# Kernel optimization log

Measured on AMD Instinct MI355X. Metric: run time of the kernel, lower is better.

## Reference

```python
import jax, jax.numpy as jnp
import numpy as np

N, C, H, E = 10000, 128, 256, 320000
CUTOFF = 5.0
EPS = 1e-5


def _ln(x, g, b):
    mu = jnp.mean(x, axis=-1, keepdims=True)
    var = jnp.var(x, axis=-1, keepdims=True)
    return (x - mu) * jax.lax.rsqrt(var + EPS) * g + b


def setup_inputs() -> dict:
    key = jax.random.key(0)
    ks = jax.random.split(key, 24)

    def w(k, shape, fan_in):
        return (jax.random.normal(k, shape, dtype=jnp.float32) / np.sqrt(fan_in)).astype(jnp.float32)

    inp = {}
    inp["x"] = jax.random.normal(ks[0], (N, 3), dtype=jnp.float32)
    inp["h"] = jax.random.normal(ks[1], (N, C), dtype=jnp.float32)
    inp["edge_index"] = jax.random.randint(ks[2], (2, E), 0, N, dtype=jnp.int32)
    # edge_mlp: Linear(2C+1 -> H), SiLU, Linear(H -> H), SiLU
    inp["We1"] = w(ks[3], (2 * C + 1, H), 2 * C + 1); inp["be1"] = jnp.zeros((H,), jnp.float32)
    inp["We2"] = w(ks[4], (H, H), H);                inp["be2"] = jnp.zeros((H,), jnp.float32)
    # node_mlp: Linear(C+H -> H), SiLU, Linear(H -> C)
    inp["Wn1"] = w(ks[5], (C + H, H), C + H);        inp["bn1"] = jnp.zeros((H,), jnp.float32)
    inp["Wn2"] = w(ks[6], (H, C), H);                inp["bn2"] = jnp.zeros((C,), jnp.float32)
    # residual mlp: Linear(C -> H), SiLU, Dropout(eval), Linear(H -> C)
    inp["Wm1"] = w(ks[7], (C, H), C);                inp["bm1"] = jnp.zeros((H,), jnp.float32)
    inp["Wm2"] = w(ks[8], (H, C), H);                inp["bm2"] = jnp.zeros((C,), jnp.float32)
    # layernorms
    inp["g1"] = jnp.ones((C,), jnp.float32); inp["beta1"] = jnp.zeros((C,), jnp.float32)
    inp["g2"] = jnp.ones((C,), jnp.float32); inp["beta2"] = jnp.zeros((C,), jnp.float32)
    return inp


def reference(x, h, edge_index, We1, be1, We2, be2, Wn1, bn1, Wn2, bn2,
              Wm1, bm1, Wm2, bm2, g1, beta1, g2, beta2):
    row, col = edge_index[0], edge_index[1]

    h_res = h
    hn = _ln(h, g1, beta1)                              # [N, C]

    # ---- EGNN layer ----
    rel = x[row] - x[col]                               # [E, 3]
    dist = jnp.linalg.norm(rel, axis=-1, keepdims=True) # [E, 1]
    edge_in = jnp.concatenate([hn[row], hn[col], dist], axis=-1)  # [E, 2C+1]
    m = jax.nn.silu(edge_in @ We1 + be1)
    m = jax.nn.silu(m @ We2 + be2)                      # [E, H]

    d = dist[:, 0]
    Ccut = 0.5 * (jnp.cos(d * jnp.pi / CUTOFF) + 1.0)
    Ccut = Ccut * (d <= CUTOFF) * (d >= 0.0)
    m = m * Ccut[:, None]

    # mean-aggregate messages at target nodes (edge_index[1])
    sums = jax.ops.segment_sum(m, col, num_segments=N)          # [N, H]
    cnt = jax.ops.segment_sum(jnp.ones((m.shape[0],), m.dtype), col, num_segments=N)
    m_aggr = sums / jnp.maximum(cnt, 1.0)[:, None]

    hd = jax.nn.silu(jnp.concatenate([hn, m_aggr], axis=-1) @ Wn1 + bn1) @ Wn2 + bn2
    h_egnn = hn + hd

    h1 = h_res + h_egnn

    # ---- norm2 + MLP residual (dropout = identity in eval) ----
    h2 = _ln(h1, g2, beta2)
    h2 = jax.nn.silu(h2 @ Wm1 + bm1) @ Wm2 + bm2
    return h1 + h2
```

## Files before the change

### kernel.cpp

```cpp
#include <hip/hip_runtime.h>

#define NN 10000
#define CC 128
#define HH 256
#define EE 320000
#define ETILE 96
#define EBLOCKS 3334

typedef __bf16 bf16_t;
typedef __bf16 bf16x8 __attribute__((ext_vector_type(8)));
typedef __bf16 bf16x4 __attribute__((ext_vector_type(4)));
typedef float f32x4 __attribute__((ext_vector_type(4)));

__device__ __forceinline__ float silu_f(float v) {
#if __has_builtin(__builtin_amdgcn_rcpf)
  return v * __builtin_amdgcn_rcpf(1.0f + __expf(-v));
#else
  return v / (1.0f + __expf(-v));
#endif
}

template<int RE, int KD, int SA, int NT>
__device__ __forceinline__ void gemm_lg(const bf16_t* sAa, const bf16_t* __restrict__ BT,
                                        int nwavebase, int lr, int quad, f32x4 acc[RE][NT]) {
  for (int kk = 0; kk < KD; kk += 32) {
    bf16x8 a[RE]; bf16x8 b[NT];
#pragma unroll
    for (int re = 0; re < RE; re++)
      a[re] = *(const bf16x8*)(sAa + (re * 16 + lr) * SA + kk + quad * 8);
#pragma unroll
    for (int ce = 0; ce < NT; ce++)
      b[ce] = *(const bf16x8*)(BT + (size_t)(nwavebase + ce * 16 + lr) * KD + kk + quad * 8);
#pragma unroll
    for (int re = 0; re < RE; re++)
#pragma unroll
      for (int ce = 0; ce < NT; ce++)
        acc[re][ce] = __builtin_amdgcn_mfma_f32_16x16x32_bf16(a[re], b[ce], acc[re][ce], 0, 0, 0);
  }
}

__global__ __launch_bounds__(256) void prep_kernel(
    const float* __restrict__ We1, const float* __restrict__ We2,
    const float* __restrict__ Wn1, const float* __restrict__ Wn2,
    const float* __restrict__ Wm1, const float* __restrict__ Wm2,
    bf16_t* __restrict__ We1T, bf16_t* __restrict__ We2T,
    bf16_t* __restrict__ Wn1T, bf16_t* __restrict__ Wn2T,
    bf16_t* __restrict__ Wm1T, bf16_t* __restrict__ Wm2T,
    float* __restrict__ sums, int* __restrict__ cnt, uint4* __restrict__ edat) {
  int i = blockIdx.x * 256 + threadIdx.x;
  if (i < 327680) {
    const float* src; bf16_t* dst; int K, Nc, idx;
    if      (i < 65536)  { src = We1; dst = We1T; K = 256; Nc = 256; idx = i; }
    else if (i < 131072) { src = We2; dst = We2T; K = 256; Nc = 256; idx = i - 65536; }
    else if (i < 229376) { src = Wn1; dst = Wn1T; K = 384; Nc = 256; idx = i - 131072; }
    else if (i < 262144) { src = Wn2; dst = Wn2T; K = 256; Nc = 128; idx = i - 229376; }
    else if (i < 294912) { src = Wm1; dst = Wm1T; K = 128; Nc = 256; idx = i - 262144; }
    else                 { src = Wm2; dst = Wm2T; K = 256; Nc = 128; idx = i - 294912; }
    int n = idx / K, k = idx - n * K;
    dst[idx] = (bf16_t)src[(size_t)k * Nc + n];
  } else if (i < 327680 + 640000) {
    f32x4 z = {0.f, 0.f, 0.f, 0.f};
    ((f32x4*)sums)[i - 327680] = z;
  } else if (i < 327680 + 640000 + 2500) {
    int4 z = {0, 0, 0, 0};
    ((int4*)cnt)[i - 967680] = z;
  } else if (i < 327680 + 640000 + 2500 + 64) {
    uint4 z = {0u, 0u, 0u, 0u};
    edat[EE + (i - 970180)] = z;
  }
}

__global__ __launch_bounds__(256, 4) void node_pre_kernel(
    const float* __restrict__ h, const float* __restrict__ g1,
    const float* __restrict__ bt1,
    const bf16_t* __restrict__ We1T, const float* __restrict__ be1,
    bf16_t* __restrict__ hn16, bf16_t* __restrict__ PQ) {
  __shared__ __align__(16) bf16_t sHn[16 * 136];
  int tid = threadIdx.x;
  int lane = tid & 63, wave = tid >> 6;
  int lr = lane & 15, quad = lane >> 4;
  int n0 = blockIdx.x * 16;

  {
    int node = tid >> 4, c0 = (tid & 15) * 8;
    size_t base = (size_t)(n0 + node) * CC;
    f32x4 u0 = *(const f32x4*)(h + base + c0);
    f32x4 u1 = *(const f32x4*)(h + base + c0 + 4);
    float s = 0.f, sq = 0.f;
#pragma unroll
    for (int j = 0; j < 4; j++) { s += u0[j] + u1[j]; sq += u0[j] * u0[j] + u1[j] * u1[j]; }
#pragma unroll
    for (int o = 8; o > 0; o >>= 1) { s += __shfl_xor(s, o); sq += __shfl_xor(sq, o); }
    float mu = s * (1.0f / CC);
    float var = sq * (1.0f / CC) - mu * mu;
    float rs = rsqrtf(var + 1e-5f);
    f32x4 gg0 = *(const f32x4*)(g1 + c0), gg1 = *(const f32x4*)(g1 + c0 + 4);
    f32x4 bb0 = *(const f32x4*)(bt1 + c0), bb1 = *(const f32x4*)(bt1 + c0 + 4);
    bf16x8 ov;
#pragma unroll
    for (int j = 0; j < 4; j++) {
      ov[j] = (bf16_t)((u0[j] - mu) * rs * gg0[j] + bb0[j]);
      ov[j + 4] = (bf16_t)((u1[j] - mu) * rs * gg1[j] + bb1[j]);
    }
    *(bf16x8*)(sHn + node * 136 + c0) = ov;
    *(bf16x8*)(hn16 + base + c0) = ov;
  }
  __syncthreads();

  bool isQ = wave >= 2;
  int rbase = (wave & 1) * 128;
  int koff = isQ ? 128 : 0;
  f32x4 zf = {0.f, 0.f, 0.f, 0.f};
  f32x4 acc[8];
#pragma unroll
  for (int i = 0; i < 8; i++) acc[i] = zf;
  for (int kk = 0; kk < 128; kk += 32) {
    bf16x8 b = *(const bf16x8*)(sHn + lr * 136 + kk + quad * 8);
    bf16x8 a[8];
#pragma unroll
    for (int re = 0; re < 8; re++)
      a[re] = *(const bf16x8*)(We1T + (size_t)(rbase + re * 16 + lr) * 256 + koff + kk + quad * 8);
#pragma unroll
    for (int re = 0; re < 8; re++)
      acc[re] = __builtin_amdgcn_mfma_f32_16x16x32_bf16(a[re], b, acc[re], 0, 0, 0);
  }
#pragma unroll
  for (int re = 0; re < 8; re++) {
    int cb = rbase + re * 16 + quad * 4;
    f32x4 bb = isQ ? zf : *(const f32x4*)(be1 + cb);
    bf16x4 o;
#pragma unroll
    for (int r = 0; r < 4; r++) o[r] = (bf16_t)(acc[re][r] + bb[r]);
    *(bf16x4*)(PQ + (size_t)(n0 + lr) * 512 + (isQ ? 256 : 0) + cb) = o;
  }
}

__global__ __launch_bounds__(256) void count_kernel(const int* __restrict__ ei, int* __restrict__ cnt) {
  int e = blockIdx.x * 256 + threadIdx.x;
  atomicAdd(&cnt[ei[EE + e]], 1);
}

__global__ __launch_bounds__(1024) void scan_kernel(const int* __restrict__ cnt, int* __restrict__ cursor) {
  __shared__ int wsum[16];
  int tid = threadIdx.x, wave = tid >> 6, lane = tid & 63;
  int base = tid * 10;
  int v[10]; int S = 0;
#pragma unroll
  for (int j = 0; j < 10; j++) {
    int i = base + j;
    v[j] = (i < NN) ? cnt[i] : 0;
    S += v[j];
  }
  int s = S;
#pragma unroll
  for (int off = 1; off < 64; off <<= 1) { int t = __shfl_up(s, off); if (lane >= off) s += t; }
  if (lane == 63) wsum[wave] = s;
  __syncthreads();
  if (tid < 16) {
    int ws = wsum[tid];
#pragma unroll
    for (int off = 1; off < 16; off <<= 1) { int t = __shfl_up(ws, off); if (tid >= off) ws += t; }
    wsum[tid] = ws;
  }
  __syncthreads();
  int ex = ((wave > 0) ? wsum[wave - 1] : 0) + s - S;
#pragma unroll
  for (int j = 0; j < 10; j++) {
    int i = base + j;
    if (i < NN) cursor[i] = ex;
    ex += v[j];
  }
}

__global__ __launch_bounds__(256) void scatter_kernel(const int* __restrict__ ei,
                                                      const float* __restrict__ x,
                                                      int* __restrict__ cursor,
                                                      uint4* __restrict__ edat) {
  int e = blockIdx.x * 256 + threadIdx.x;
  int r = ei[e], c = ei[EE + e];
  float dx = x[3 * r] - x[3 * c];
  float dy = x[3 * r + 1] - x[3 * c + 1];
  float dz = x[3 * r + 2] - x[3 * c + 2];
  float d = sqrtf(dx * dx + dy * dy + dz * dz);
  float cc = (d <= 5.0f) ? 0.5f * (cosf(d * 0.6283185307179586f) + 1.0f) : 0.0f;
  int pos = atomicAdd(&cursor[c], 1);
  uint4 v = {(unsigned)r, (unsigned)c, __float_as_uint(d), __float_as_uint(cc)};
  edat[pos] = v;
}

__global__ __launch_bounds__(256, 3) void edge_mlp_kernel(
    const uint4* __restrict__ edat, const bf16_t* __restrict__ PQ,
    const float* __restrict__ We1last,
    const bf16_t* __restrict__ We2T, const float* __restrict__ be2,
    float* __restrict__ sums, int blk0) {
  __shared__ __align__(16) bf16_t sM1[ETILE * 264];
  __shared__ int sRow[ETILE], sCol[ETILE];
  __shared__ float sD[ETILE], sCc[ETILE];
  __shared__ unsigned long long sMaskA;
  __shared__ unsigned sMaskB;
  int tid = threadIdx.x;
  int lane = tid & 63, wave = tid >> 6;
  int lr = lane & 15, quad = lane >> 4;
  int e0 = (blk0 + blockIdx.x) * ETILE;

  if (tid < ETILE) {
    uint4 v = edat[e0 + tid];
    sRow[tid] = (int)v.x; sCol[tid] = (int)v.y;
    sD[tid] = __uint_as_float(v.z); sCc[tid] = __uint_as_float(v.w);
  }
  __syncthreads();

  if (tid < ETILE) {
    int fl = (tid > 0) && (sCol[tid] != sCol[tid - 1]);
    unsigned long long m = __ballot(fl);
    if (tid == 0) sMaskA = m;
    if (tid == 64) sMaskB = (unsigned)m;
  }

#pragma unroll
  for (int i = 0; i < ETILE * 32 / 256; i++) {
    int o = tid + i * 256;
    int e = o >> 5, q = o & 31;
    int k0 = q * 8;
    int row = sRow[e], col = sCol[e];
    float d = sD[e];
    bf16x8 pv = *(const bf16x8*)(PQ + (size_t)row * 512 + k0);
    bf16x8 qv = *(const bf16x8*)(PQ + (size_t)col * 512 + 256 + k0);
    f32x4 wl0 = *(const f32x4*)(We1last + k0);
    f32x4 wl1 = *(const f32x4*)(We1last + k0 + 4);
    bf16x8 m;
#pragma unroll
    for (int j = 0; j < 4; j++) {
      m[j] = (bf16_t)silu_f((float)pv[j] + (float)qv[j] + d * wl0[j]);
      m[j + 4] = (bf16_t)silu_f((float)pv[j + 4] + (float)qv[j + 4] + d * wl1[j]);
    }
    *(bf16x8*)(sM1 + e * 264 + k0) = m;
  }
  __syncthreads();

  f32x4 zf = {0.f, 0.f, 0.f, 0.f};
  f32x4 acc[6][4];
#pragma unroll
  for (int i = 0; i < 6; i++)
#pragma unroll
    for (int j = 0; j < 4; j++) acc[i][j] = zf;
  gemm_lg<6, 256, 264, 4>(sM1, We2T, wave * 64, lr, quad, acc);

  float be2v[4];
#pragma unroll
  for (int ce = 0; ce < 4; ce++) be2v[ce] = be2[wave * 64 + ce * 16 + lr];
#pragma unroll
  for (int re = 0; re < 6; re++) {
    f32x4 cc = *(const f32x4*)(sCc + re * 16 + quad * 4);
#pragma unroll
    for (int ce = 0; ce < 4; ce++)
#pragma unroll
      for (int r = 0; r < 4; r++)
        acc[re][ce][r] = silu_f(acc[re][ce][r] + be2v[ce]) * cc[r];
  }

  {
    unsigned long long mA = sMaskA;
    unsigned long long mB = (unsigned long long)sMaskB;
    int lo = 0;
    while (lo < ETILE) {
      int hi;
      if (lo < 63) {
        unsigned long long t = mA & (~0ull << (lo + 1));
        hi = t ? (__ffsll((long long)t) - 1)
               : (mB ? 64 + __ffsll((long long)mB) - 1 : ETILE);
      } else {
        unsigned long long t1 = mB & (~0ull << (lo - 63));
        hi = t1 ? 64 + __ffsll((long long)t1) - 1 : ETILE;
      }
      f32x4 tv = zf;
#pragma unroll
      for (int re = 0; re < 6; re++) {
        int t0 = re * 16, t1e = t0 + 16;
        if (t1e <= lo || t0 >= hi) continue;
        if (t0 >= lo && t1e <= hi) {
#pragma unroll
          for (int r = 0; r < 4; r++)
#pragma unroll
            for (int ce = 0; ce < 4; ce++)
              tv[ce] += acc[re][ce][r];
        } else {
          int eb = t0 + quad * 4;
#pragma unroll
          for (int r = 0; r < 4; r++) {
            int e = eb + r;
            bool in = (e >= lo) && (e < hi);
#pragma unroll
            for (int ce = 0; ce < 4; ce++)
              tv[ce] += in ? acc[re][ce][r] : 0.0f;
          }
        }
      }
#pragma unroll
      for (int ce = 0; ce < 4; ce++) {
        tv[ce] += __shfl_xor(tv[ce], 16);
        tv[ce] += __shfl_xor(tv[ce], 32);
      }
      if (quad == 0) {
        int colv = sCol[lo];
#pragma unroll
        for (int ce = 0; ce < 4; ce++)
          atomicAdd(&sums[(size_t)colv * HH + wave * 64 + ce * 16 + lr], tv[ce]);
      }
      lo = hi;
    }
  }
}

__global__ __launch_bounds__(256, 2) void node_fused_kernel(
    const float* __restrict__ h, const bf16_t* __restrict__ hn16,
    const float* __restrict__ sums, const int* __restrict__ cnt,
    const bf16_t* __restrict__ Wn1T, const float* __restrict__ bn1,
    const bf16_t* __restrict__ Wn2T, const float* __restrict__ bn2,
    const float* __restrict__ g2, const float* __restrict__ bt2,
    const bf16_t* __restrict__ Wm1T, const float* __restrict__ bm1,
    const bf16_t* __restrict__ Wm2T, const float* __restrict__ bm2,
    float* __restrict__ out) {
  __shared__ __align__(16) bf16_t sA1[32 * 392];
  __shared__ __align__(16) bf16_t sM[32 * 264];
  __shared__ __align__(16) float sH1[32 * 132];
  __shared__ __align__(16) bf16_t sLn[32 * 136];
  __shared__ float sRc[32];
  int tid = threadIdx.x;
  int lane = tid & 63, wave = tid >> 6;
  int lr = lane & 15, quad = lane >> 4;
  int n0 = blockIdx.x * 32;

  if (tid < 32) {
    int node = n0 + tid;
    sRc[tid] = (node < NN) ? 1.0f / fmaxf((float)cnt[node], 1.0f) : 0.0f;
  }
  __syncthreads();

#pragma unroll
  for (int i = 0; i < 6; i++) {
    int o = tid + i * 256;
    int e = o / 48, q = o - e * 48;
    int node = n0 + e;
    if (q < 16) {
      uint4 v = {0u, 0u, 0u, 0u};
      if (node < NN) v = *(const uint4*)(hn16 + (size_t)node * CC + q * 8);
      *(uint4*)(sA1 + e * 392 + q * 8) = v;
    } else {
      bf16x8 bv = {};
      if (node < NN) {
        float rc = sRc[e];
        const float* sp = sums + (size_t)node * HH + (q - 16) * 8;
#pragma unroll
        for (int k2 = 0; k2 < 8; k2++) bv[k2] = (bf16_t)(sp[k2] * rc);
      }
      *(bf16x8*)(sA1 + e * 392 + 128 + (q - 16) * 8) = bv;
    }
  }
  __syncthreads();

  f32x4 zf = {0.f, 0.f, 0.f, 0.f};
  {
    f32x4 acc[2][4];
#pragma unroll
    for (int i = 0; i < 2; i++)
#pragma unroll
      for (int j = 0; j < 4; j++) acc[i][j] = zf;
    gemm_lg<2, 384, 392, 4>(sA1, Wn1T, wave * 64, lr, quad, acc);
#pragma unroll
    for (int ce = 0; ce < 4; ce++) {
      int n = wave * 64 + ce * 16 + lr;
      float b1 = bn1[n];
#pragma unroll
      for (int re = 0; re < 2; re++)
#pragma unroll
        for (int r = 0; r < 4; r++)
          sM[(re * 16 + quad * 4 + r) * 264 + n] = (bf16_t)silu_f(acc[re][ce][r] + b1);
    }
  }
  __syncthreads();

  {
    f32x4 acc[2][2];
#pragma unroll
    for (int i = 0; i < 2; i++) { acc[i][0] = zf; acc[i][1] = zf; }
    gemm_lg<2, 256, 264, 2>(sM, Wn2T, wave * 32, lr, quad, acc);
#pragma unroll
    for (int ce = 0; ce < 2; ce++) {
      int n = wave * 32 + ce * 16 + lr;
      float b2 = bn2[n];
#pragma unroll
      for (int re = 0; re < 2; re++)
#pragma unroll
        for (int r = 0; r < 4; r++) {
          int node = re * 16 + quad * 4 + r;
          float hv = 0.f;
          if (n0 + node < NN) hv = h[(size_t)(n0 + node) * CC + n];
          sH1[node * 132 + n] = hv + (float)sA1[node * 392 + n] + acc[re][ce][r] + b2;
        }
    }
  }
  __syncthreads();

  {
    int node = tid >> 3, c0 = (tid & 7) * 16;
    f32x4 u[4];
    float s = 0.f, sq = 0.f;
#pragma unroll
    for (int j = 0; j < 4; j++) {
      u[j] = *(const f32x4*)(sH1 + node * 132 + c0 + j * 4);
#pragma unroll
      for (int r = 0; r < 4; r++) { s += u[j][r]; sq += u[j][r] * u[j][r]; }
    }
    s += __shfl_xor(s, 1); sq += __shfl_xor(sq, 1);
    s += __shfl_xor(s, 2); sq += __shfl_xor(sq, 2);
    s += __shfl_xor(s, 4); sq += __shfl_xor(sq, 4);
    float mu = s * (1.0f / CC);
    float var = sq * (1.0f / CC) - mu * mu;
    float rs = rsqrtf(var + 1e-5f);
#pragma unroll
    for (int j2 = 0; j2 < 2; j2++) {
      f32x4 gg0 = *(const f32x4*)(g2 + c0 + j2 * 8);
      f32x4 gg1 = *(const f32x4*)(g2 + c0 + j2 * 8 + 4);
      f32x4 bb0 = *(const f32x4*)(bt2 + c0 + j2 * 8);
      f32x4 bb1 = *(const f32x4*)(bt2 + c0 + j2 * 8 + 4);
      bf16x8 ov;
#pragma unroll
      for (int r = 0; r < 4; r++) {
        ov[r] = (bf16_t)((u[j2 * 2][r] - mu) * rs * gg0[r] + bb0[r]);
        ov[r + 4] = (bf16_t)((u[j2 * 2 + 1][r] - mu) * rs * gg1[r] + bb1[r]);
      }
      *(bf16x8*)(sLn + node * 136 + c0 + j2 * 8) = ov;
    }
  }
  __syncthreads();

  {
    f32x4 acc[2][4];
#pragma unroll
    for (int i = 0; i < 2; i++)
#pragma unroll
      for (int j = 0; j < 4; j++) acc[i][j] = zf;
    gemm_lg<2, 128, 136, 4>(sLn, Wm1T, wave * 64, lr, quad, acc);
#pragma unroll
    for (int ce = 0; ce < 4; ce++) {
      int n = wave * 64 + ce * 16 + lr;
      float b1 = bm1[n];
#pragma unroll
      for (int re = 0; re < 2; re++)
#pragma unroll
        for (int r = 0; r < 4; r++)
          sM[(re * 16 + quad * 4 + r) * 264 + n] = (bf16_t)silu_f(acc[re][ce][r] + b1);
    }
  }
  __syncthreads();

  {
    f32x4 acc[2][2];
#pragma unroll
    for (int i = 0; i < 2; i++) { acc[i][0] = zf; acc[i][1] = zf; }
    gemm_lg<2, 256, 264, 2>(sM, Wm2T, wave * 32, lr, quad, acc);
#pragma unroll
    for (int ce = 0; ce < 2; ce++) {
      int n = wave * 32 + ce * 16 + lr;
      float b2 = bm2[n];
#pragma unroll
      for (int re = 0; re < 2; re++)
#pragma unroll
        for (int r = 0; r < 4; r++) {
          int node = re * 16 + quad * 4 + r;
          if (n0 + node < NN)
            out[(size_t)(n0 + node) * CC + n] = sH1[node * 132 + n] + acc[re][ce][r] + b2;
        }
    }
  }
}

extern "C" void kernel_launch(void* const* d_in, const int* in_sizes, int n_in,
                              void* d_out, int out_size, void* d_ws, size_t ws_size,
                              hipStream_t stream) {
  const float* x    = (const float*)d_in[0];
  const float* h    = (const float*)d_in[1];
  const int*   ei   = (const int*)d_in[2];
  const float* We1  = (const float*)d_in[3];
  const float* be1  = (const float*)d_in[4];
  const float* We2  = (const float*)d_in[5];
  const float* be2  = (const float*)d_in[6];
  const float* Wn1  = (const float*)d_in[7];
  const float* bn1  = (const float*)d_in[8];
  const float* Wn2  = (const float*)d_in[9];
  const float* bn2  = (const float*)d_in[10];
  const float* Wm1  = (const float*)d_in[11];
  const float* bm1  = (const float*)d_in[12];
  const float* Wm2  = (const float*)d_in[13];
  const float* bm2  = (const float*)d_in[14];
  const float* g1   = (const float*)d_in[15];
  const float* bt1  = (const float*)d_in[16];
  const float* g2   = (const float*)d_in[17];
  const float* bt2  = (const float*)d_in[18];
  float* out = (float*)d_out;

  char* wp = (char*)d_ws;
  size_t off = 0;
  auto alloc = [&](size_t bytes) -> void* {
    void* p = wp + off;
    off = (off + bytes + 255) & ~(size_t)255;
    return p;
  };

  bf16_t* hn16   = (bf16_t*)alloc((size_t)NN * CC * 2);
  bf16_t* PQ     = (bf16_t*)alloc((size_t)NN * 512 * 2);
  float*  sums   = (float*)alloc((size_t)NN * HH * 4);
  int*    cnt    = (int*)alloc((size_t)NN * 4);
  int*    cursor = (int*)alloc((size_t)NN * 4);
  uint4*  edat   = (uint4*)alloc((size_t)(EBLOCKS * ETILE) * 16);
  bf16_t* We1T   = (bf16_t*)alloc(256 * 256 * 2);
  bf16_t* We2T   = (bf16_t*)alloc(256 * 256 * 2);
  bf16_t* Wn1T   = (bf16_t*)alloc(256 * 384 * 2);
  bf16_t* Wn2T   = (bf16_t*)alloc(128 * 256 * 2);
  bf16_t* Wm1T   = (bf16_t*)alloc(256 * 128 * 2);
  bf16_t* Wm2T   = (bf16_t*)alloc(128 * 256 * 2);

  prep_kernel<<<3791, 256, 0, stream>>>(We1, We2, Wn1, Wn2, Wm1, Wm2,
                                        We1T, We2T, Wn1T, Wn2T, Wm1T, Wm2T,
                                        sums, cnt, edat);

  node_pre_kernel<<<NN / 16, 256, 0, stream>>>(h, g1, bt1, We1T, be1, hn16, PQ);

  count_kernel<<<EE / 256, 256, 0, stream>>>(ei, cnt);
  scan_kernel<<<1, 1024, 0, stream>>>(cnt, cursor);
  scatter_kernel<<<EE / 256, 256, 0, stream>>>(ei, x, cursor, edat);

  edge_mlp_kernel<<<1112, 256, 0, stream>>>(edat, PQ, We1 + 256 * 256,
                                            We2T, be2, sums, 0);
  edge_mlp_kernel<<<1112, 256, 0, stream>>>(edat, PQ, We1 + 256 * 256,
                                            We2T, be2, sums, 1112);
  edge_mlp_kernel<<<1110, 256, 0, stream>>>(edat, PQ, We1 + 256 * 256,
                                            We2T, be2, sums, 2224);

  node_fused_kernel<<<(NN + 31) / 32, 256, 0, stream>>>(h, hn16, sums, cnt,
                                                        Wn1T, bn1, Wn2T, bn2,
                                                        g2, bt2, Wm1T, bm1, Wm2T, bm2, out);
}
```

Measured before the change: 311.7 us.

## Use 512-thread edge MLP blocks with 8 waves splitting output columns

The edge MLP kernel now runs 512 threads per block, so 8 waves each compute 32 output columns of the second GEMM instead of 4 waves computing 64. The generic gemm_lg helper is replaced by an inline MFMA 16x16x32 loop. The three split launches are merged into one launch over all edge tiles. This lowers per-thread accumulator pressure and raises occupancy, at the cost of each wave re-reading the shared A tile and issuing more atomics per segment.

```diff
diff --git a/kernel.cpp b/kernel.cpp
--- a/kernel.cpp
+++ b/kernel.cpp
@@ -188,11 +188,11 @@
   edat[pos] = v;
 }
 
-__global__ __launch_bounds__(256, 3) void edge_mlp_kernel(
+__global__ __launch_bounds__(512, 4) void edge_mlp_kernel(
     const uint4* __restrict__ edat, const bf16_t* __restrict__ PQ,
     const float* __restrict__ We1last,
     const bf16_t* __restrict__ We2T, const float* __restrict__ be2,
-    float* __restrict__ sums, int blk0) {
+    float* __restrict__ sums) {
   __shared__ __align__(16) bf16_t sM1[ETILE * 264];
   __shared__ int sRow[ETILE], sCol[ETILE];
   __shared__ float sD[ETILE], sCc[ETILE];
@@ -201,7 +201,7 @@
   int tid = threadIdx.x;
   int lane = tid & 63, wave = tid >> 6;
   int lr = lane & 15, quad = lane >> 4;
-  int e0 = (blk0 + blockIdx.x) * ETILE;
+  int e0 = blockIdx.x * ETILE;
 
   if (tid < ETILE) {
     uint4 v = edat[e0 + tid];
@@ -217,9 +217,9 @@
     if (tid == 64) sMaskB = (unsigned)m;
   }
 
-#pragma unroll
-  for (int i = 0; i < ETILE * 32 / 256; i++) {
-    int o = tid + i * 256;
+#pragma unroll 3
+  for (int i = 0; i < 6; i++) {
+    int o = tid + i * 512;
     int e = o >> 5, q = o & 31;
     int k0 = q * 8;
     int row = sRow[e], col = sCol[e];
@@ -239,21 +239,32 @@
   __syncthreads();
 
   f32x4 zf = {0.f, 0.f, 0.f, 0.f};
-  f32x4 acc[6][4];
-#pragma unroll
-  for (int i = 0; i < 6; i++)
-#pragma unroll
-    for (int j = 0; j < 4; j++) acc[i][j] = zf;
-  gemm_lg<6, 256, 264, 4>(sM1, We2T, wave * 64, lr, quad, acc);
-
-  float be2v[4];
-#pragma unroll
-  for (int ce = 0; ce < 4; ce++) be2v[ce] = be2[wave * 64 + ce * 16 + lr];
+  f32x4 acc[6][2];
+#pragma unroll
+  for (int i = 0; i < 6; i++) { acc[i][0] = zf; acc[i][1] = zf; }
+  for (int kk = 0; kk < 256; kk += 32) {
+    bf16x8 a[6]; bf16x8 b[2];
+#pragma unroll
+    for (int re = 0; re < 6; re++)
+      a[re] = *(const bf16x8*)(sM1 + (re * 16 + lr) * 264 + kk + quad * 8);
+#pragma unroll
+    for (int ce = 0; ce < 2; ce++)
+      b[ce] = *(const bf16x8*)(We2T + (size_t)(wave * 32 + ce * 16 + lr) * 256 + kk + quad * 8);
+#pragma unroll
+    for (int re = 0; re < 6; re++)
+#pragma unroll
+      for (int ce = 0; ce < 2; ce++)
+        acc[re][ce] = __builtin_amdgcn_mfma_f32_16x16x32_bf16(a[re], b[ce], acc[re][ce], 0, 0, 0);
+  }
+
+  float be2v[2];
+#pragma unroll
+  for (int ce = 0; ce < 2; ce++) be2v[ce] = be2[wave * 32 + ce * 16 + lr];
 #pragma unroll
   for (int re = 0; re < 6; re++) {
     f32x4 cc = *(const f32x4*)(sCc + re * 16 + quad * 4);
 #pragma unroll
-    for (int ce = 0; ce < 4; ce++)
+    for (int ce = 0; ce < 2; ce++)
 #pragma unroll
       for (int r = 0; r < 4; r++)
         acc[re][ce][r] = silu_f(acc[re][ce][r] + be2v[ce]) * cc[r];
@@ -273,39 +284,31 @@
         unsigned long long t1 = mB & (~0ull << (lo - 63));
         hi = t1 ? 64 + __ffsll((long long)t1) - 1 : ETILE;
       }
-      f32x4 tv = zf;
+      float tv0 = 0.f, tv1 = 0.f;
 #pragma unroll
       for (int re = 0; re < 6; re++) {
         int t0 = re * 16, t1e = t0 + 16;
         if (t1e <= lo || t0 >= hi) continue;
         if (t0 >= lo && t1e <= hi) {
 #pragma unroll
-          for (int r = 0; r < 4; r++)
-#pragma unroll
-            for (int ce = 0; ce < 4; ce++)
-              tv[ce] += acc[re][ce][r];
+          for (int r = 0; r < 4; r++) { tv0 += acc[re][0][r]; tv1 += acc[re][1][r]; }
         } else {
           int eb = t0 + quad * 4;
 #pragma unroll
           for (int r = 0; r < 4; r++) {
             int e = eb + r;
             bool in = (e >= lo) && (e < hi);
-#pragma unroll
-            for (int ce = 0; ce < 4; ce++)
-              tv[ce] += in ? acc[re][ce][r] : 0.0f;
+            tv0 += in ? acc[re][0][r] : 0.0f;
+            tv1 += in ? acc[re][1][r] : 0.0f;
           }
         }
       }
-#pragma unroll
-      for (int ce = 0; ce < 4; ce++) {
-        tv[ce] += __shfl_xor(tv[ce], 16);
-        tv[ce] += __shfl_xor(tv[ce], 32);
-      }
+      tv0 += __shfl_xor(tv0, 16); tv0 += __shfl_xor(tv0, 32);
+      tv1 += __shfl_xor(tv1, 16); tv1 += __shfl_xor(tv1, 32);
       if (quad == 0) {
         int colv = sCol[lo];
-#pragma unroll
-        for (int ce = 0; ce < 4; ce++)
-          atomicAdd(&sums[(size_t)colv * HH + wave * 64 + ce * 16 + lr], tv[ce]);
+        atomicAdd(&sums[(size_t)colv * HH + wave * 32 + lr], tv0);
+        atomicAdd(&sums[(size_t)colv * HH + wave * 32 + 16 + lr], tv1);
       }
       lo = hi;
     }
@@ -531,12 +534,8 @@
   scan_kernel<<<1, 1024, 0, stream>>>(cnt, cursor);
   scatter_kernel<<<EE / 256, 256, 0, stream>>>(ei, x, cursor, edat);
 
-  edge_mlp_kernel<<<1112, 256, 0, stream>>>(edat, PQ, We1 + 256 * 256,
-                                            We2T, be2, sums, 0);
-  edge_mlp_kernel<<<1112, 256, 0, stream>>>(edat, PQ, We1 + 256 * 256,
-                                            We2T, be2, sums, 1112);
-  edge_mlp_kernel<<<1110, 256, 0, stream>>>(edat, PQ, We1 + 256 * 256,
-                                            We2T, be2, sums, 2224);
+  edge_mlp_kernel<<<EBLOCKS, 512, 0, stream>>>(edat, PQ, We1 + 256 * 256,
+                                               We2T, be2, sums);
 
   node_fused_kernel<<<(NN + 31) / 32, 256, 0, stream>>>(h, hn16, sums, cnt,
                                                         Wn1T, bn1, Wn2T, bn2,
```

After: 296.9 us. 1.05x faster.
